# Kernel optimization log

Hardware: AMD Instinct MI355X
Metric: run time of the kernel (lower is better)

The kernel has to match this reference:

```python
import math
import jax, jax.numpy as jnp
import numpy as np

MAX_T = 300
B, T, V, D, H = 16, 256, 25, 128, 8


def _layernorm(x, g, b):
    m = x.mean(-1, keepdims=True)
    var = ((x - m) ** 2).mean(-1, keepdims=True)
    return (x - m) / jnp.sqrt(var + 1e-5) * g + b


def setup_inputs() -> dict:
    key = jax.random.key(0)
    ks = jax.random.split(key, 8)
    d = D // H
    init = lambda k, shape: jax.random.normal(k, shape, dtype=jnp.float32) * 0.02
    return dict(
        x=jax.random.normal(ks[0], (B, T, V, D), dtype=jnp.float32),
        ln1_g=jnp.ones((D,), jnp.float32), ln1_b=jnp.zeros((D,), jnp.float32),
        qkv_w=init(ks[1], (D, 3 * D)), qkv_b=jnp.zeros((3 * D,), jnp.float32),
        proj_w=init(ks[2], (D, D)), proj_b=jnp.zeros((D,), jnp.float32),
        logit_scale=jnp.full((H, 1, 1), math.log(math.sqrt(d)), dtype=jnp.float32),
        rel_pos_bias=init(ks[3], (H, 2 * MAX_T - 1)),
        ln2_g=jnp.ones((D,), jnp.float32), ln2_b=jnp.zeros((D,), jnp.float32),
        ffn_w1=init(ks[4], (D, 4 * D)), ffn_b1=jnp.zeros((4 * D,), jnp.float32),
        ffn_w2=init(ks[5], (4 * D, D)), ffn_b2=jnp.zeros((D,), jnp.float32),
    )


def reference(x, ln1_g, ln1_b, qkv_w, qkv_b, proj_w, proj_b, logit_scale,
              rel_pos_bias, ln2_g, ln2_b, ffn_w1, ffn_b1, ffn_w2, ffn_b2):
    b, t, v_, dm = x.shape
    h = logit_scale.shape[0]
    d = dm // h
    # (B, T, V, D) -> (B*V, T, D): attention runs over frames per joint
    xf = x.transpose(0, 2, 1, 3).reshape(b * v_, t, dm)
    res = xf
    xn = _layernorm(xf, ln1_g, ln1_b)
    qkv = (xn @ qkv_w + qkv_b).reshape(b * v_, t, 3, h, d).transpose(2, 0, 3, 1, 4)
    q, k, v = qkv[0], qkv[1], qkv[2]  # (BV, h, T, d)
    scale = jnp.exp(jnp.minimum(logit_scale, math.log(100.0)))  # (h,1,1)
    qn = q / jnp.maximum(jnp.linalg.norm(q, axis=-1, keepdims=True), 1e-12) * scale
    kn = k / jnp.maximum(jnp.linalg.norm(k, axis=-1, keepdims=True), 1e-12)
    # learned relative-position bias, gathered to (h, T, T)
    coords = jnp.arange(t)
    rel = coords[:, None] - coords[None, :] + (MAX_T - 1)
    bias = rel_pos_bias[:, rel]
    # SDPA applies its default 1/sqrt(head_dim) scale on top of logit_scale
    scores = jnp.einsum('bhtd,bhsd->bhts', qn, kn) / math.sqrt(d) + bias[None]
    attn = jax.nn.softmax(scores, axis=-1)
    out = jnp.einsum('bhts,bhsd->bhtd', attn, v)
    out = out.transpose(0, 2, 1, 3).reshape(b * v_, t, dm)
    xf = res + (out @ proj_w + proj_b)
    y = _layernorm(xf, ln2_g, ln2_b)
    y = jax.nn.gelu(y @ ffn_w1 + ffn_b1, approximate=False) @ ffn_w2 + ffn_b2
    xf = xf + y
    return xf.reshape(b, v_, t, dm).transpose(0, 2, 1, 3)
```

## Files before the change

### kernel.cpp

```cpp
#include <hip/hip_runtime.h>
#include <hip/hip_fp16.h>
#include <math.h>

#define B_   16
#define T_   256
#define V_   25
#define D_   128
#define H_   8
#define DH   16
#define BV_  (B_*V_)
#define MAXT 300
#define NREL (2*MAXT-1)

typedef __attribute__((ext_vector_type(8))) short short8;
typedef __attribute__((ext_vector_type(4))) float f32x4;
typedef __attribute__((ext_vector_type(4))) _Float16 half4;
typedef __attribute__((ext_vector_type(8))) _Float16 half8;

__device__ inline short f2bf(float f) {
  union { float f; unsigned u; } a; a.f = f;
  unsigned r = (a.u + 0x7FFF + ((a.u >> 16) & 1)) >> 16;
  return (short)r;
}

__device__ inline float gelu_fast(float u) {
  float s = u * fmaf(0.0713548162726f, u*u, 1.5957691216057f);
  return u * __builtin_amdgcn_rcpf(1.0f + __expf(-s));
}

__global__ __launch_bounds__(256) void k0_prep(
    const float* __restrict__ qkv_w, const float* __restrict__ pw,
    const float* __restrict__ w1,    const float* __restrict__ w2,
    short* __restrict__ qkv_wt, short* __restrict__ pwt,
    _Float16* __restrict__ w1t, _Float16* __restrict__ w2t)
{
  int i = blockIdx.x*256 + threadIdx.x;
  if (i < 384*128) { int n = i >> 7, k = i & 127; qkv_wt[i] = f2bf(qkv_w[k*384 + n]); }
  if (i < 128*128) { int n = i >> 7, k = i & 127; pwt[i]    = f2bf(pw[k*128 + n]); }
  if (i < 512*128) { int n = i >> 7, k = i & 127; w1t[i]    = (_Float16)w1[k*512 + n]; }
  if (i < 128*512) {
    int r = i & 3, lane = (i >> 2) & 63, hn = (i >> 8) & 31, ot = i >> 13;
    int k = hn*16 + (lane >> 4)*4 + r;
    int n = ot*16 + (lane & 15);
    w2t[i] = (_Float16)w2[k*128 + n];
  }
}

__global__ __launch_bounds__(256) void k1_ln_qkv(
    const float* __restrict__ x, const float* __restrict__ g1, const float* __restrict__ b1,
    const short* __restrict__ qkv_wt, const float* __restrict__ qkv_b,
    const float* __restrict__ logit_scale,
    _Float16* __restrict__ qb, _Float16* __restrict__ kb, _Float16* __restrict__ vt)
{
  __shared__ short xn[64][136];
  const int tid = threadIdx.x;
  const int bv  = blockIdx.x / (T_/64);
  const int t0  = (blockIdx.x % (T_/64)) * 64;
  const int b   = bv / V_, v = bv % V_;

  {
    const int j = tid & 15;
    float4 gA = *(const float4*)(g1 + j*8), gB = *(const float4*)(g1 + j*8 + 4);
    float4 bA = *(const float4*)(b1 + j*8), bB = *(const float4*)(b1 + j*8 + 4);
    float gg[8] = {gA.x,gA.y,gA.z,gA.w,gB.x,gB.y,gB.z,gB.w};
    float bb[8] = {bA.x,bA.y,bA.z,bA.w,bB.x,bB.y,bB.z,bB.w};
    for (int rep = 0; rep < 4; ++rep) {
      const int tok = rep*16 + (tid >> 4);
      const float* xp = x + (((size_t)b*T_ + (t0+tok))*V_ + v)*D_ + j*8;
      float4 a0 = *(const float4*)xp;
      float4 a1 = *(const float4*)(xp+4);
      float e[8] = {a0.x,a0.y,a0.z,a0.w,a1.x,a1.y,a1.z,a1.w};
      float s = 0.f;
      #pragma unroll
      for (int q = 0; q < 8; ++q) s += e[q];
      #pragma unroll
      for (int m = 1; m < 16; m <<= 1) s += __shfl_xor(s, m, 16);
      float mean = s * (1.0f/128.0f);
      float s2 = 0.f;
      #pragma unroll
      for (int q = 0; q < 8; ++q) { float d = e[q]-mean; s2 += d*d; }
      #pragma unroll
      for (int m = 1; m < 16; m <<= 1) s2 += __shfl_xor(s2, m, 16);
      float rstd = rsqrtf(s2*(1.0f/128.0f) + 1e-5f);
      short8 o;
      #pragma unroll
      for (int q = 0; q < 8; ++q) o[q] = f2bf((e[q]-mean)*rstd*gg[q] + bb[q]);
      *(short8*)&xn[tok][j*8] = o;
    }
  }
  __syncthreads();

  const int wave = tid >> 6, lane = tid & 63;
  const int col = lane & 15, quad = lane >> 4;
  short8 af[4][4];
  #pragma unroll
  for (int tt = 0; tt < 4; ++tt)
    #pragma unroll
    for (int kk = 0; kk < 4; ++kk)
      af[tt][kk] = *(const short8*)&xn[tt*16+col][kk*32 + quad*8];

  for (int it = 0; it < 6; ++it) {
    const int tile = wave*6 + it;
    const int n0 = tile*16;
    short8 bf[4];
    #pragma unroll
    for (int kk = 0; kk < 4; ++kk)
      bf[kk] = *(const short8*)(qkv_wt + (size_t)(n0+col)*128 + kk*32 + quad*8);
    f32x4 acc[4] = {{0.f,0.f,0.f,0.f},{0.f,0.f,0.f,0.f},{0.f,0.f,0.f,0.f},{0.f,0.f,0.f,0.f}};
    #pragma unroll
    for (int kk = 0; kk < 4; ++kk)
      #pragma unroll
      for (int tt = 0; tt < 4; ++tt)
        acc[tt] = __builtin_amdgcn_mfma_f32_16x16x32_bf16(af[tt][kk], bf[kk], acc[tt], 0, 0, 0);
    const float bias = qkv_b[n0+col];
    const int h = tile & 7;
    const size_t bh = (size_t)bv*H_ + h;
    if (tile < 16) {
      const float scale = (tile < 8)
        ? __expf(fminf(logit_scale[h], 4.605170185988091f)) * 0.25f : 1.0f;
      #pragma unroll
      for (int tt = 0; tt < 4; ++tt) {
        float val[4], inv[4];
        #pragma unroll
        for (int r = 0; r < 4; ++r) {
          val[r] = acc[tt][r] + bias;
          float s = val[r]*val[r];
          #pragma unroll
          for (int m = 1; m < 16; m <<= 1) s += __shfl_xor(s, m, 16);
          inv[r] = 1.0f / fmaxf(sqrtf(s), 1e-12f);
        }
        const size_t obase = (bh*T_ + (t0 + tt*16 + quad*4))*DH + col;
        if (tile < 8) {
          #pragma unroll
          for (int r = 0; r < 4; ++r) qb[obase + (size_t)r*DH] = (_Float16)(val[r]*inv[r]*scale);
        } else {
          #pragma unroll
          for (int r = 0; r < 4; ++r) kb[obase + (size_t)r*DH] = (_Float16)(val[r]*inv[r]);
        }
      }
    } else {
      #pragma unroll
      for (int tt = 0; tt < 4; ++tt) {
        half4 vh;
        #pragma unroll
        for (int r = 0; r < 4; ++r) vh[r] = (_Float16)(acc[tt][r] + bias);
        *(half4*)(vt + bh*4096 + (size_t)(t0/16 + tt)*256 + col*16 + quad*4) = vh;
      }
    }
  }
}

__global__ __launch_bounds__(256) void k2_attn(
    const float* __restrict__ rel_pos_bias,
    const _Float16* __restrict__ qb, const _Float16* __restrict__ kb,
    const _Float16* __restrict__ vt, float* __restrict__ xattn)
{
  __shared__ float bias_s[NREL + 1];
  const int tid = threadIdx.x;
  const int bh  = blockIdx.x;
  const int h   = bh & (H_-1);
  const int bv  = bh >> 3;
  for (int j = tid; j < NREL; j += 256) bias_s[j] = rel_pos_bias[h*NREL + j];
  __syncthreads();

  const int wave = tid >> 6, lane = tid & 63;
  const int nn = lane & 15, quad = lane >> 4;
  const size_t qkbase = (size_t)bh * (T_*DH);
  const size_t vbase  = (size_t)bh * 4096;

  half4 qf[4];
  #pragma unroll
  for (int tt = 0; tt < 4; ++tt)
    qf[tt] = *(const half4*)(qb + qkbase + (size_t)(wave*64 + tt*16 + nn)*DH + quad*4);

  f32x4 o[4];
  #pragma unroll
  for (int tt = 0; tt < 4; ++tt) o[tt] = (f32x4){0.f,0.f,0.f,0.f};
  float lsum[4] = {0.f,0.f,0.f,0.f};

  half4 kf = *(const half4*)(kb + qkbase + (size_t)nn*DH + quad*4);
  half4 vf = *(const half4*)(vt + vbase + (size_t)nn*16 + quad*4);

  for (int s16 = 0; s16 < 16; ++s16) {
    half4 kf_n, vf_n;
    if (s16 < 15) {
      kf_n = *(const half4*)(kb + qkbase + (size_t)((s16+1)*16 + nn)*DH + quad*4);
      vf_n = *(const half4*)(vt + vbase + (size_t)(s16+1)*256 + nn*16 + quad*4);
    }
    #pragma unroll
    for (int tt = 0; tt < 4; ++tt) {
      f32x4 c = {0.f,0.f,0.f,0.f};
      c = __builtin_amdgcn_mfma_f32_16x16x16f16(kf, qf[tt], c, 0, 0, 0);
      const int ib = (wave*64 + tt*16 + nn) - (s16*16 + quad*4) + (MAXT-1);
      half4 pa;
      #pragma unroll
      for (int r = 0; r < 4; ++r) {
        float p = __expf(c[r] + bias_s[ib - r]);
        lsum[tt] += p;
        pa[r] = (_Float16)p;
      }
      o[tt] = __builtin_amdgcn_mfma_f32_16x16x16f16(pa, vf, o[tt], 0, 0, 0);
    }
    kf = kf_n; vf = vf_n;
  }

  #pragma unroll
  for (int tt = 0; tt < 4; ++tt) {
    float l = lsum[tt];
    l += __shfl_xor(l, 16);
    l += __shfl_xor(l, 32);
    float rinv = 1.0f / l;
    #pragma unroll
    for (int r = 0; r < 4; ++r) {
      float inv = __shfl(rinv, quad*4 + r, 16);
      const int t = wave*64 + tt*16 + quad*4 + r;
      xattn[((size_t)bv*T_ + t)*D_ + h*DH + nn] = o[tt][r] * inv;
    }
  }
}

__global__ __launch_bounds__(256) void k3_proj(
    const float* __restrict__ x, const short* __restrict__ pwt,
    const float* __restrict__ proj_b, float* __restrict__ xf2)
{
  __shared__ short a_s[64][136];
  const int tid = threadIdx.x;
  const int bv  = blockIdx.x / (T_/64);
  const int t0  = (blockIdx.x % (T_/64)) * 64;
  const int b   = bv / V_, v = bv % V_;

  {
    const int j = tid & 15;
    for (int rep = 0; rep < 4; ++rep) {
      const int tok = rep*16 + (tid >> 4);
      const float* ap = xf2 + ((size_t)bv*T_ + t0+tok)*D_ + j*8;
      float4 a0 = *(const float4*)ap;
      float4 a1 = *(const float4*)(ap+4);
      float e[8] = {a0.x,a0.y,a0.z,a0.w,a1.x,a1.y,a1.z,a1.w};
      short8 o;
      #pragma unroll
      for (int q = 0; q < 8; ++q) o[q] = f2bf(e[q]);
      *(short8*)&a_s[tok][j*8] = o;
    }
  }
  __syncthreads();

  const int wave = tid >> 6, lane = tid & 63;
  const int col = lane & 15, quad = lane >> 4;
  short8 af[4][4];
  #pragma unroll
  for (int tt = 0; tt < 4; ++tt)
    #pragma unroll
    for (int kk = 0; kk < 4; ++kk)
      af[tt][kk] = *(const short8*)&a_s[tt*16+col][kk*32 + quad*8];

  for (int it = 0; it < 2; ++it) {
    const int n0 = (wave*2 + it)*16;
    short8 bf[4];
    #pragma unroll
    for (int kk = 0; kk < 4; ++kk)
      bf[kk] = *(const short8*)(pwt + (size_t)(n0+col)*128 + kk*32 + quad*8);
    f32x4 acc[4] = {{0.f,0.f,0.f,0.f},{0.f,0.f,0.f,0.f},{0.f,0.f,0.f,0.f},{0.f,0.f,0.f,0.f}};
    #pragma unroll
    for (int kk = 0; kk < 4; ++kk)
      #pragma unroll
      for (int tt = 0; tt < 4; ++tt)
        acc[tt] = __builtin_amdgcn_mfma_f32_16x16x32_bf16(af[tt][kk], bf[kk], acc[tt], 0, 0, 0);
    const float pbv = proj_b[n0+col];
    #pragma unroll
    for (int tt = 0; tt < 4; ++tt)
      #pragma unroll
      for (int r = 0; r < 4; ++r) {
        const int t = t0 + tt*16 + quad*4 + r;
        float res = x[(((size_t)b*T_ + t)*V_ + v)*D_ + n0 + col];
        xf2[((size_t)bv*T_ + t)*D_ + n0 + col] = acc[tt][r] + pbv + res;
      }
  }
}

__global__ __launch_bounds__(256) void k4_ffn(
    const float* __restrict__ xf2, const float* __restrict__ g2, const float* __restrict__ b2,
    const _Float16* __restrict__ w1t, const float* __restrict__ fb1,
    const _Float16* __restrict__ w2t, const float* __restrict__ fb2,
    float* __restrict__ out)
{
  __shared__ __align__(16) char smem[128*136*2];
  _Float16 (*y_s)[136] = (_Float16 (*)[136])smem;
  _Float16 (*w1c)[136] = (_Float16 (*)[136])smem;
  _Float16 *w2c = (_Float16*)(smem + 64*136*2);

  const int tid = threadIdx.x;
  const int bv  = blockIdx.x / (T_/128);
  const int t0  = (blockIdx.x % (T_/128)) * 128;
  const int b   = bv / V_, v = bv % V_;

  half8 p_w1[4], p_w2[4];
  #pragma unroll
  for (int j = 0; j < 4; ++j) {
    const int u = j*256 + tid;
    p_w1[j] = *(const half8*)(w1t + (size_t)(u >> 4)*128 + (u & 15)*8);
    p_w2[j] = *(const half8*)(w2t + (size_t)((u >> 7)*32 + ((u >> 5) & 3))*256 + (u & 31)*8);
  }

  {
    const int j = tid & 15;
    float4 gA = *(const float4*)(g2 + j*8), gB = *(const float4*)(g2 + j*8 + 4);
    float4 bA = *(const float4*)(b2 + j*8), bB = *(const float4*)(b2 + j*8 + 4);
    float gg[8] = {gA.x,gA.y,gA.z,gA.w,gB.x,gB.y,gB.z,gB.w};
    float bb[8] = {bA.x,bA.y,bA.z,bA.w,bB.x,bB.y,bB.z,bB.w};
    for (int rep = 0; rep < 8; ++rep) {
      const int tok = rep*16 + (tid >> 4);
      const float* xp = xf2 + ((size_t)bv*T_ + t0+tok)*D_ + j*8;
      float4 a0 = *(const float4*)xp;
      float4 a1 = *(const float4*)(xp+4);
      float e[8] = {a0.x,a0.y,a0.z,a0.w,a1.x,a1.y,a1.z,a1.w};
      float s = 0.f;
      #pragma unroll
      for (int q = 0; q < 8; ++q) s += e[q];
      #pragma unroll
      for (int m = 1; m < 16; m <<= 1) s += __shfl_xor(s, m, 16);
      float mean = s * (1.0f/128.0f);
      float s2 = 0.f;
      #pragma unroll
      for (int q = 0; q < 8; ++q) { float d = e[q]-mean; s2 += d*d; }
      #pragma unroll
      for (int m = 1; m < 16; m <<= 1) s2 += __shfl_xor(s2, m, 16);
      float rstd = rsqrtf(s2*(1.0f/128.0f) + 1e-5f);
      half8 o;
      #pragma unroll
      for (int q = 0; q < 8; ++q) o[q] = (_Float16)((e[q]-mean)*rstd*gg[q] + bb[q]);
      *(half8*)&y_s[tok][j*8] = o;
    }
  }
  __syncthreads();

  const int wave = tid >> 6, lane = tid & 63;
  const int col = lane & 15, quad = lane >> 4;

  half8 yf[2][4];
  #pragma unroll
  for (int tt = 0; tt < 2; ++tt)
    #pragma unroll
    for (int kk = 0; kk < 4; ++kk)
      yf[tt][kk] = *(const half8*)&y_s[wave*32 + tt*16 + col][kk*32 + quad*8];
  __syncthreads();

  f32x4 acc2[2][8];
  #pragma unroll
  for (int tt = 0; tt < 2; ++tt)
    #pragma unroll
    for (int ot = 0; ot < 8; ++ot) acc2[tt][ot] = (f32x4){0.f,0.f,0.f,0.f};

  for (int c = 0; c < 8; ++c) {
    #pragma unroll
    for (int j = 0; j < 4; ++j) {
      const int u = j*256 + tid;
      *(half8*)&w1c[u >> 4][(u & 15)*8] = p_w1[j];
      *(half8*)&w2c[(size_t)u*8]        = p_w2[j];
    }
    __syncthreads();

    if (c < 7) {
      #pragma unroll
      for (int j = 0; j < 4; ++j) {
        const int u = j*256 + tid;
        p_w1[j] = *(const half8*)(w1t + (size_t)((c+1)*64 + (u >> 4))*128 + (u & 15)*8);
        p_w2[j] = *(const half8*)(w2t + (size_t)((u >> 7)*32 + (c+1)*4 + ((u >> 5) & 3))*256 + (u & 31)*8);
      }
    }

    #pragma unroll
    for (int ht = 0; ht < 4; ++ht) {
      half8 w1f[4];
      #pragma unroll
      for (int kk = 0; kk < 4; ++kk)
        w1f[kk] = *(const half8*)&w1c[ht*16+col][kk*32 + quad*8];
      f32x4 c0 = {0.f,0.f,0.f,0.f}, c1 = {0.f,0.f,0.f,0.f};
      #pragma unroll
      for (int kk = 0; kk < 4; ++kk) {
        c0 = __builtin_amdgcn_mfma_f32_16x16x32_f16(w1f[kk], yf[0][kk], c0, 0, 0, 0);
        c1 = __builtin_amdgcn_mfma_f32_16x16x32_f16(w1f[kk], yf[1][kk], c1, 0, 0, 0);
      }
      const int hn = c*4 + ht;
      const f32x4 b1v = *(const f32x4*)(fb1 + hn*16 + quad*4);
      half4 pa0, pa1;
      #pragma unroll
      for (int r = 0; r < 4; ++r) {
        pa0[r] = (_Float16)gelu_fast(c0[r] + b1v[r]);
        pa1[r] = (_Float16)gelu_fast(c1[r] + b1v[r]);
      }
      #pragma unroll
      for (int ot = 0; ot < 8; ++ot) {
        half4 w2f = *(const half4*)&w2c[((ot*4 + ht)*64 + lane)*4];
        acc2[0][ot] = __builtin_amdgcn_mfma_f32_16x16x16f16(pa0, w2f, acc2[0][ot], 0, 0, 0);
        acc2[1][ot] = __builtin_amdgcn_mfma_f32_16x16x16f16(pa1, w2f, acc2[1][ot], 0, 0, 0);
      }
    }
    __syncthreads();
  }

  const int tw = t0 + wave*32;
  #pragma unroll
  for (int tt = 0; tt < 2; ++tt)
    #pragma unroll
    for (int ot = 0; ot < 8; ++ot) {
      const float bo = fb2[ot*16 + col];
      #pragma unroll
      for (int r = 0; r < 4; ++r) {
        const int t = tw + tt*16 + quad*4 + r;
        float val = acc2[tt][ot][r] + bo + xf2[((size_t)bv*T_ + t)*D_ + ot*16 + col];
        out[(((size_t)b*T_ + t)*V_ + v)*D_ + ot*16 + col] = val;
      }
    }
}

extern "C" void kernel_launch(void* const* d_in, const int* in_sizes, int n_in,
                              void* d_out, int out_size, void* d_ws, size_t ws_size,
                              hipStream_t stream)
{
  (void)in_sizes; (void)n_in; (void)out_size; (void)ws_size;
  const float* x     = (const float*)d_in[0];
  const float* g1    = (const float*)d_in[1];
  const float* b1    = (const float*)d_in[2];
  const float* qkv_w = (const float*)d_in[3];
  const float* qkv_b = (const float*)d_in[4];
  const float* pw    = (const float*)d_in[5];
  const float* pb    = (const float*)d_in[6];
  const float* ls    = (const float*)d_in[7];
  const float* rpb   = (const float*)d_in[8];
  const float* g2    = (const float*)d_in[9];
  const float* b2    = (const float*)d_in[10];
  const float* w1    = (const float*)d_in[11];
  const float* fb1   = (const float*)d_in[12];
  const float* w2    = (const float*)d_in[13];
  const float* fb2   = (const float*)d_in[14];
  float* out = (float*)d_out;

  const size_t n = (size_t)BV_*T_*D_;
  char* ws = (char*)d_ws;
  _Float16* qb  = (_Float16*)ws;
  _Float16* kb  = (_Float16*)(ws + n*2);
  float*    xf2 = (float*)(ws + n*4);
  _Float16* vt  = (_Float16*)(ws + n*8);
  short*    qkv_wt = (short*)(ws + n*10);
  short*    pwt    = qkv_wt + 384*128;
  _Float16* w1t    = (_Float16*)(pwt + 128*128);
  _Float16* w2t    = w1t + 512*128;

  k0_prep  <<<256,          dim3(256), 0, stream>>>(qkv_w, pw, w1, w2, qkv_wt, pwt, w1t, w2t);
  k1_ln_qkv<<<BV_*(T_/64),  dim3(256), 0, stream>>>(x, g1, b1, qkv_wt, qkv_b, ls, qb, kb, vt);
  k2_attn  <<<BV_*H_,       dim3(256), 0, stream>>>(rpb, qb, kb, vt, xf2);
  k3_proj  <<<BV_*(T_/64),  dim3(256), 0, stream>>>(x, pwt, pb, xf2);
  k4_ffn   <<<BV_*(T_/128), dim3(256), 0, stream>>>(xf2, g2, b2, w1t, fb1, w2t, fb2, out);
}
```

Before: 325.8 us.

## Fuse output projection and residual into FFN kernel, keeping xf2 in registers

Merges the projection kernel into the FFN kernel. Each block converts its 128-token tile of attention output to bf16 in shared memory, runs the projection MFMAs with the residual and bias preloaded into the accumulators, and computes LayerNorm2 directly from those register accumulators. The fp32 xf2 intermediate is no longer written and re-read through global memory, and one launch disappears. In exchange the FFN kernel holds 64 more accumulator registers per thread, which may lower occupancy, and the LayerNorm now uses cross-lane shuffles and scalar fp16 stores to shared memory.

```diff
diff --git a/kernel.cpp b/kernel.cpp
--- a/kernel.cpp
+++ b/kernel.cpp
@@ -219,80 +219,91 @@
   }
 }
 
-__global__ __launch_bounds__(256) void k3_proj(
-    const float* __restrict__ x, const short* __restrict__ pwt,
-    const float* __restrict__ proj_b, float* __restrict__ xf2)
-{
-  __shared__ short a_s[64][136];
-  const int tid = threadIdx.x;
-  const int bv  = blockIdx.x / (T_/64);
-  const int t0  = (blockIdx.x % (T_/64)) * 64;
-  const int b   = bv / V_, v = bv % V_;
-
-  {
-    const int j = tid & 15;
-    for (int rep = 0; rep < 4; ++rep) {
-      const int tok = rep*16 + (tid >> 4);
-      const float* ap = xf2 + ((size_t)bv*T_ + t0+tok)*D_ + j*8;
-      float4 a0 = *(const float4*)ap;
-      float4 a1 = *(const float4*)(ap+4);
-      float e[8] = {a0.x,a0.y,a0.z,a0.w,a1.x,a1.y,a1.z,a1.w};
-      short8 o;
-      #pragma unroll
-      for (int q = 0; q < 8; ++q) o[q] = f2bf(e[q]);
-      *(short8*)&a_s[tok][j*8] = o;
-    }
-  }
-  __syncthreads();
-
-  const int wave = tid >> 6, lane = tid & 63;
-  const int col = lane & 15, quad = lane >> 4;
-  short8 af[4][4];
-  #pragma unroll
-  for (int tt = 0; tt < 4; ++tt)
-    #pragma unroll
-    for (int kk = 0; kk < 4; ++kk)
-      af[tt][kk] = *(const short8*)&a_s[tt*16+col][kk*32 + quad*8];
-
-  for (int it = 0; it < 2; ++it) {
-    const int n0 = (wave*2 + it)*16;
-    short8 bf[4];
-    #pragma unroll
-    for (int kk = 0; kk < 4; ++kk)
-      bf[kk] = *(const short8*)(pwt + (size_t)(n0+col)*128 + kk*32 + quad*8);
-    f32x4 acc[4] = {{0.f,0.f,0.f,0.f},{0.f,0.f,0.f,0.f},{0.f,0.f,0.f,0.f},{0.f,0.f,0.f,0.f}};
-    #pragma unroll
-    for (int kk = 0; kk < 4; ++kk)
-      #pragma unroll
-      for (int tt = 0; tt < 4; ++tt)
-        acc[tt] = __builtin_amdgcn_mfma_f32_16x16x32_bf16(af[tt][kk], bf[kk], acc[tt], 0, 0, 0);
-    const float pbv = proj_b[n0+col];
-    #pragma unroll
-    for (int tt = 0; tt < 4; ++tt)
-      #pragma unroll
-      for (int r = 0; r < 4; ++r) {
-        const int t = t0 + tt*16 + quad*4 + r;
-        float res = x[(((size_t)b*T_ + t)*V_ + v)*D_ + n0 + col];
-        xf2[((size_t)bv*T_ + t)*D_ + n0 + col] = acc[tt][r] + pbv + res;
-      }
-  }
-}
-
-__global__ __launch_bounds__(256) void k4_ffn(
-    const float* __restrict__ xf2, const float* __restrict__ g2, const float* __restrict__ b2,
+__global__ __launch_bounds__(256) void k34_ffn(
+    const float* __restrict__ x, const float* __restrict__ xattn,
+    const short* __restrict__ pwt, const float* __restrict__ proj_b,
+    const float* __restrict__ g2, const float* __restrict__ b2,
     const _Float16* __restrict__ w1t, const float* __restrict__ fb1,
     const _Float16* __restrict__ w2t, const float* __restrict__ fb2,
     float* __restrict__ out)
 {
-  __shared__ __align__(16) char smem[128*136*2];
+  __shared__ __align__(16) char smem[34816];
+  short    (*a_s)[136] = (short (*)[136])smem;
   _Float16 (*y_s)[136] = (_Float16 (*)[136])smem;
   _Float16 (*w1c)[136] = (_Float16 (*)[136])smem;
-  _Float16 *w2c = (_Float16*)(smem + 64*136*2);
+  _Float16 *w2c        = (_Float16*)(smem + 17408);
 
   const int tid = threadIdx.x;
-  const int bv  = blockIdx.x / (T_/128);
-  const int t0  = (blockIdx.x % (T_/128)) * 128;
+  const int bv  = blockIdx.x >> 1;
+  const int t0  = (blockIdx.x & 1) * 128;
   const int b   = bv / V_, v = bv % V_;
+  const int wave = tid >> 6, lane = tid & 63;
+  const int col = lane & 15, quad = lane >> 4;
+  const int tw  = t0 + wave*32;
+
+  f32x4 accA[2][8];
+  #pragma unroll
+  for (int tt = 0; tt < 2; ++tt)
+    #pragma unroll
+    for (int ot = 0; ot < 8; ++ot) {
+      const float pbv = proj_b[ot*16 + col];
+      #pragma unroll
+      for (int r = 0; r < 4; ++r) {
+        const int t = tw + tt*16 + quad*4 + r;
+        accA[tt][ot][r] = x[(((size_t)b*T_ + t)*V_ + v)*D_ + ot*16 + col] + pbv;
+      }
+    }
+
+  {
+    const int j = tid & 15, trow = tid >> 4;
+    const float* ap = xattn + ((size_t)bv*T_ + t0 + trow)*D_ + j*8;
+    float4 a0 = *(const float4*)ap;
+    float4 a1 = *(const float4*)(ap+4);
+    for (int rep = 0; rep < 8; ++rep) {
+      float4 n0, n1;
+      if (rep < 7) {
+        const float* np = ap + (size_t)(rep+1)*16*D_;
+        n0 = *(const float4*)np; n1 = *(const float4*)(np+4);
+      }
+      float e[8] = {a0.x,a0.y,a0.z,a0.w,a1.x,a1.y,a1.z,a1.w};
+      short8 o;
+      #pragma unroll
+      for (int q = 0; q < 8; ++q) o[q] = f2bf(e[q]);
+      *(short8*)&a_s[rep*16 + trow][j*8] = o;
+      a0 = n0; a1 = n1;
+    }
+  }
+  __syncthreads();
+
+  short8 af[2][4];
+  #pragma unroll
+  for (int tt = 0; tt < 2; ++tt)
+    #pragma unroll
+    for (int kk = 0; kk < 4; ++kk)
+      af[tt][kk] = *(const short8*)&a_s[wave*32 + tt*16 + col][kk*32 + quad*8];
+
+  {
+    short8 bf[4];
+    #pragma unroll
+    for (int kk = 0; kk < 4; ++kk)
+      bf[kk] = *(const short8*)(pwt + (size_t)col*128 + kk*32 + quad*8);
+    #pragma unroll
+    for (int ot = 0; ot < 8; ++ot) {
+      short8 bfn[4];
+      if (ot < 7)
+        #pragma unroll
+        for (int kk = 0; kk < 4; ++kk)
+          bfn[kk] = *(const short8*)(pwt + (size_t)((ot+1)*16+col)*128 + kk*32 + quad*8);
+      #pragma unroll
+      for (int kk = 0; kk < 4; ++kk) {
+        accA[0][ot] = __builtin_amdgcn_mfma_f32_16x16x32_bf16(af[0][kk], bf[kk], accA[0][ot], 0, 0, 0);
+        accA[1][ot] = __builtin_amdgcn_mfma_f32_16x16x32_bf16(af[1][kk], bf[kk], accA[1][ot], 0, 0, 0);
+      }
+      if (ot < 7)
+        #pragma unroll
+        for (int kk = 0; kk < 4; ++kk) bf[kk] = bfn[kk];
+    }
+  }
 
   half8 p_w1[4], p_w2[4];
   #pragma unroll
@@ -303,39 +314,31 @@
   }
 
   {
-    const int j = tid & 15;
-    float4 gA = *(const float4*)(g2 + j*8), gB = *(const float4*)(g2 + j*8 + 4);
-    float4 bA = *(const float4*)(b2 + j*8), bB = *(const float4*)(b2 + j*8 + 4);
-    float gg[8] = {gA.x,gA.y,gA.z,gA.w,gB.x,gB.y,gB.z,gB.w};
-    float bb[8] = {bA.x,bA.y,bA.z,bA.w,bB.x,bB.y,bB.z,bB.w};
-    for (int rep = 0; rep < 8; ++rep) {
-      const int tok = rep*16 + (tid >> 4);
-      const float* xp = xf2 + ((size_t)bv*T_ + t0+tok)*D_ + j*8;
-      float4 a0 = *(const float4*)xp;
-      float4 a1 = *(const float4*)(xp+4);
-      float e[8] = {a0.x,a0.y,a0.z,a0.w,a1.x,a1.y,a1.z,a1.w};
-      float s = 0.f;
-      #pragma unroll
-      for (int q = 0; q < 8; ++q) s += e[q];
-      #pragma unroll
-      for (int m = 1; m < 16; m <<= 1) s += __shfl_xor(s, m, 16);
-      float mean = s * (1.0f/128.0f);
-      float s2 = 0.f;
-      #pragma unroll
-      for (int q = 0; q < 8; ++q) { float d = e[q]-mean; s2 += d*d; }
-      #pragma unroll
-      for (int m = 1; m < 16; m <<= 1) s2 += __shfl_xor(s2, m, 16);
-      float rstd = rsqrtf(s2*(1.0f/128.0f) + 1e-5f);
-      half8 o;
-      #pragma unroll
-      for (int q = 0; q < 8; ++q) o[q] = (_Float16)((e[q]-mean)*rstd*gg[q] + bb[q]);
-      *(half8*)&y_s[tok][j*8] = o;
-    }
-  }
-  __syncthreads();
-
-  const int wave = tid >> 6, lane = tid & 63;
-  const int col = lane & 15, quad = lane >> 4;
+    float gg[8], bb[8];
+    #pragma unroll
+    for (int ot = 0; ot < 8; ++ot) { gg[ot] = g2[ot*16 + col]; bb[ot] = b2[ot*16 + col]; }
+    #pragma unroll
+    for (int tt = 0; tt < 2; ++tt)
+      #pragma unroll
+      for (int r = 0; r < 4; ++r) {
+        float s = 0.f;
+        #pragma unroll
+        for (int ot = 0; ot < 8; ++ot) s += accA[tt][ot][r];
+        #pragma unroll
+        for (int m = 1; m < 16; m <<= 1) s += __shfl_xor(s, m, 16);
+        float mean = s * (1.0f/128.0f);
+        float s2 = 0.f;
+        #pragma unroll
+        for (int ot = 0; ot < 8; ++ot) { float d = accA[tt][ot][r] - mean; s2 += d*d; }
+        #pragma unroll
+        for (int m = 1; m < 16; m <<= 1) s2 += __shfl_xor(s2, m, 16);
+        float rstd = rsqrtf(s2*(1.0f/128.0f) + 1e-5f);
+        const int row = wave*32 + tt*16 + quad*4 + r;
+        #pragma unroll
+        for (int ot = 0; ot < 8; ++ot)
+          y_s[row][ot*16 + col] = (_Float16)((accA[tt][ot][r]-mean)*rstd*gg[ot] + bb[ot]);
+      }
+  }
 
   half8 yf[2][4];
   #pragma unroll
@@ -399,7 +402,6 @@
     __syncthreads();
   }
 
-  const int tw = t0 + wave*32;
   #pragma unroll
   for (int tt = 0; tt < 2; ++tt)
     #pragma unroll
@@ -408,8 +410,7 @@
       #pragma unroll
       for (int r = 0; r < 4; ++r) {
         const int t = tw + tt*16 + quad*4 + r;
-        float val = acc2[tt][ot][r] + bo + xf2[((size_t)bv*T_ + t)*D_ + ot*16 + col];
-        out[(((size_t)b*T_ + t)*V_ + v)*D_ + ot*16 + col] = val;
+        out[(((size_t)b*T_ + t)*V_ + v)*D_ + ot*16 + col] = acc2[tt][ot][r] + bo + accA[tt][ot][r];
       }
     }
 }
@@ -440,7 +441,7 @@
   char* ws = (char*)d_ws;
   _Float16* qb  = (_Float16*)ws;
   _Float16* kb  = (_Float16*)(ws + n*2);
-  float*    xf2 = (float*)(ws + n*4);
+  float*    xattn = (float*)(ws + n*4);
   _Float16* vt  = (_Float16*)(ws + n*8);
   short*    qkv_wt = (short*)(ws + n*10);
   short*    pwt    = qkv_wt + 384*128;
@@ -449,7 +450,7 @@
 
   k0_prep  <<<256,          dim3(256), 0, stream>>>(qkv_w, pw, w1, w2, qkv_wt, pwt, w1t, w2t);
   k1_ln_qkv<<<BV_*(T_/64),  dim3(256), 0, stream>>>(x, g1, b1, qkv_wt, qkv_b, ls, qb, kb, vt);
-  k2_attn  <<<BV_*H_,       dim3(256), 0, stream>>>(rpb, qb, kb, vt, xf2);
-  k3_proj  <<<BV_*(T_/64),  dim3(256), 0, stream>>>(x, pwt, pb, xf2);
-  k4_ffn   <<<BV_*(T_/128), dim3(256), 0, stream>>>(xf2, g2, b2, w1t, fb1, w2t, fb2, out);
-}
+  k2_attn  <<<BV_*H_,       dim3(256), 0, stream>>>(rpb, qb, kb, vt, xattn);
+  k34_ffn  <<<BV_*(T_/128), dim3(256), 0, stream>>>(x, xattn, pwt, pb, g2, b2,
+                                                    w1t, fb1, w2t, fb2, out);
+}
```

Result: slower. 350.7 us (+7.6%).
